# Optimization experiments

Hardware: AMD Instinct MI355X
Metric: run time of the kernel (lower is better)

## Reference

```python
import jax, jax.numpy as jnp
import numpy as np

EXPERT_NUM = 4
TOPK = 2
HIDDEN = 512
B, S = 8, 8192


def setup_inputs() -> dict:
    key = jax.random.key(0)
    k1, k2, k3 = jax.random.split(key, 3)
    x = jax.random.normal(k1, (B, S, HIDDEN), dtype=jnp.float32)
    gate_w = jax.random.normal(k2, (EXPERT_NUM, HIDDEN), dtype=jnp.float32) * (1.0 / np.sqrt(HIDDEN))
    gate_b = jax.random.normal(k3, (EXPERT_NUM,), dtype=jnp.float32) * 0.01
    return {"x": x, "gate_w": gate_w, "gate_b": gate_b}


def reference(x, gate_w, gate_b):
    # logits: [B, S, E]
    logits = jnp.einsum("bsh,eh->bse", x, gate_w) + gate_b
    logits_topk, indices = jax.lax.top_k(logits, TOPK)  # [B,S,K]
    # scatter topk logits into -inf-filled tensor, then softmax over experts
    T = B * S
    flat_logits_topk = logits_topk.reshape(T, TOPK)
    flat_indices = indices.reshape(T, TOPK)
    neg_inf = jnp.full((T, EXPERT_NUM), -jnp.inf, dtype=logits.dtype)
    sparse = neg_inf.at[jnp.arange(T)[:, None], flat_indices].set(flat_logits_topk)
    sparse_logits = jax.nn.softmax(sparse, axis=-1).reshape(B, S, EXPERT_NUM)
    gate_logit = logits.reshape(-1, EXPERT_NUM)  # [B*S, E]
    return sparse_logits, indices, gate_logit
```

## Files before the change

### kernel.cpp

```cpp
#include <hip/hip_runtime.h>
#include <math.h>

#define HIDDEN  512
#define EXPERTS 4

__global__ __launch_bounds__(256, 4) void gating_kernel(
    const float* __restrict__ x,
    const float* __restrict__ gate_w,
    const float* __restrict__ gate_b,
    float* __restrict__ out_sparse,
    float* __restrict__ out_idx,
    float* __restrict__ out_logit,
    int T)
{
    const int lane   = threadIdx.x & 63;
    const int wave   = (int)((blockIdx.x * blockDim.x + threadIdx.x) >> 6);
    const int nwaves = (int)((gridDim.x * blockDim.x) >> 6);

    float4 gw0[EXPERTS], gw1[EXPERTS];
#pragma unroll
    for (int e = 0; e < EXPERTS; ++e) {
        gw0[e] = *reinterpret_cast<const float4*>(gate_w + e * HIDDEN + lane * 4);
        gw1[e] = *reinterpret_cast<const float4*>(gate_w + e * HIDDEN + 256 + lane * 4);
    }
    const float b0 = gate_b[0], b1 = gate_b[1], b2 = gate_b[2], b3 = gate_b[3];

    for (int t = wave; t < T; t += nwaves) {
        const float* xt = x + (size_t)t * HIDDEN;
        const float4 xv0 = *reinterpret_cast<const float4*>(xt + lane * 4);
        const float4 xv1 = *reinterpret_cast<const float4*>(xt + 256 + lane * 4);

        float s[EXPERTS];
#pragma unroll
        for (int e = 0; e < EXPERTS; ++e) {
            s[e] = xv0.x * gw0[e].x + xv0.y * gw0[e].y + xv0.z * gw0[e].z + xv0.w * gw0[e].w
                 + xv1.x * gw1[e].x + xv1.y * gw1[e].y + xv1.z * gw1[e].z + xv1.w * gw1[e].w;
        }

#pragma unroll
        for (int off = 32; off >= 1; off >>= 1) {
#pragma unroll
            for (int e = 0; e < EXPERTS; ++e)
                s[e] += __shfl_xor(s[e], off, 64);
        }

        const float l0 = s[0] + b0, l1 = s[1] + b1, l2 = s[2] + b2, l3 = s[3] + b3;
        const float l[4] = {l0, l1, l2, l3};

        int i1 = 0; float m1 = l[0];
#pragma unroll
        for (int e = 1; e < 4; ++e) { if (l[e] > m1) { m1 = l[e]; i1 = e; } }
        int i2 = -1; float m2 = -INFINITY;
#pragma unroll
        for (int e = 0; e < 4; ++e) { if (e != i1 && l[e] > m2) { m2 = l[e]; i2 = e; } }

        const float e2  = expf(m2 - m1);
        const float inv = 1.0f / (1.0f + e2);
        const float p1  = inv, p2 = e2 * inv;

        float sp[4];
#pragma unroll
        for (int e = 0; e < 4; ++e)
            sp[e] = (e == i1) ? p1 : ((e == i2) ? p2 : 0.0f);

        if (lane == 0) {
            const float4 spv = {sp[0], sp[1], sp[2], sp[3]};
            *reinterpret_cast<float4*>(out_sparse + (size_t)t * 4) = spv;
            const float2 iv = {(float)i1, (float)i2};
            *reinterpret_cast<float2*>(out_idx + (size_t)t * 2) = iv;
            const float4 lv = {l0, l1, l2, l3};
            *reinterpret_cast<float4*>(out_logit + (size_t)t * 4) = lv;
        }
    }
}

extern "C" void kernel_launch(void* const* d_in, const int* in_sizes, int n_in,
                              void* d_out, int out_size, void* d_ws, size_t ws_size,
                              hipStream_t stream) {
    const float* x      = (const float*)d_in[0];
    const float* gate_w = (const float*)d_in[1];
    const float* gate_b = (const float*)d_in[2];

    const int T = in_sizes[0] / HIDDEN;

    float* out_sparse = (float*)d_out;
    float* out_idx    = out_sparse + (size_t)T * EXPERTS;
    float* out_logit  = out_idx    + (size_t)T * 2;

    const dim3 block(256);
    const dim3 grid(1024);
    gating_kernel<<<grid, block, 0, stream>>>(x, gate_w, gate_b,
                                              out_sparse, out_idx, out_logit, T);
}
```

Measured before the change: 191.9 us.

## Process four tokens per wave with transpose-style butterfly reduction

Each wave now loads four token rows at once and keeps more loads in flight. The reduction first shuffles pairs of expert partial sums so that each lane holds one expert's partial. Only one value per token then goes through the remaining xor stages, which cuts the shuffle count per token from 24 to about 10. The result is redistributed with a few extra shuffles, and a tail loop handles leftover tokens. The aim is to hide memory latency in this bandwidth-bound kernel, at the cost of higher register pressure.

```diff
diff --git a/kernel.cpp b/kernel.cpp
--- a/kernel.cpp
+++ b/kernel.cpp
@@ -3,6 +3,7 @@
 
 #define HIDDEN  512
 #define EXPERTS 4
+#define QUAD    4
 
 __global__ __launch_bounds__(256, 4) void gating_kernel(
     const float* __restrict__ x,
@@ -24,52 +25,147 @@
         gw1[e] = *reinterpret_cast<const float4*>(gate_w + e * HIDDEN + 256 + lane * 4);
     }
     const float b0 = gate_b[0], b1 = gate_b[1], b2 = gate_b[2], b3 = gate_b[3];
+    const int id = lane & 3;
 
-    for (int t = wave; t < T; t += nwaves) {
+    const int nquads = T >> 2;
+
+    for (int q = wave; q < nquads; q += nwaves) {
+        const int t0 = q * 4;
+
+        float4 xv0[QUAD], xv1[QUAD];
+#pragma unroll
+        for (int j = 0; j < QUAD; ++j) {
+            const float* xt = x + (size_t)(t0 + j) * HIDDEN;
+            xv0[j] = *reinterpret_cast<const float4*>(xt + lane * 4);
+            xv1[j] = *reinterpret_cast<const float4*>(xt + 256 + lane * 4);
+        }
+
+        float s[QUAD][EXPERTS];
+#pragma unroll
+        for (int j = 0; j < QUAD; ++j) {
+#pragma unroll
+            for (int e = 0; e < EXPERTS; ++e) {
+                s[j][e] = xv0[j].x * gw0[e].x + xv0[j].y * gw0[e].y
+                        + xv0[j].z * gw0[e].z + xv0[j].w * gw0[e].w
+                        + xv1[j].x * gw1[e].x + xv1[j].y * gw1[e].y
+                        + xv1[j].z * gw1[e].z + xv1[j].w * gw1[e].w;
+            }
+        }
+
+        float u[QUAD], v[QUAD];
+#pragma unroll
+        for (int j = 0; j < QUAD; ++j) {
+            float snd = (lane & 1) ? s[j][0] : s[j][1];
+            float rcv = __shfl_xor(snd, 1, 64);
+            u[j] = ((lane & 1) ? s[j][1] : s[j][0]) + rcv;
+        }
+#pragma unroll
+        for (int j = 0; j < QUAD; ++j) {
+            float snd = (lane & 1) ? s[j][2] : s[j][3];
+            float rcv = __shfl_xor(snd, 1, 64);
+            v[j] = ((lane & 1) ? s[j][3] : s[j][2]) + rcv;
+        }
+
+        float r[QUAD];
+#pragma unroll
+        for (int j = 0; j < QUAD; ++j) {
+            float snd = (lane & 2) ? u[j] : v[j];
+            float rcv = __shfl_xor(snd, 2, 64);
+            r[j] = ((lane & 2) ? v[j] : u[j]) + rcv;
+        }
+
+#pragma unroll
+        for (int j = 0; j < QUAD; ++j) r[j] += __shfl_xor(r[j], 4, 64);
+#pragma unroll
+        for (int j = 0; j < QUAD; ++j) r[j] += __shfl_xor(r[j], 8, 64);
+#pragma unroll
+        for (int j = 0; j < QUAD; ++j) r[j] += __shfl_xor(r[j], 16, 64);
+#pragma unroll
+        for (int j = 0; j < QUAD; ++j) r[j] += __shfl_xor(r[j], 32, 64);
+
+        float ga[QUAD], gb[QUAD], gc[QUAD];
+#pragma unroll
+        for (int j = 0; j < QUAD; ++j) ga[j] = __shfl_xor(r[j], 1, 64);
+#pragma unroll
+        for (int j = 0; j < QUAD; ++j) gb[j] = __shfl_xor(r[j], 2, 64);
+#pragma unroll
+        for (int j = 0; j < QUAD; ++j) gc[j] = __shfl_xor(ga[j], 2, 64);
+
+#pragma unroll
+        for (int j = 0; j < QUAD; ++j) {
+            float l_[4];
+#pragma unroll
+            for (int e = 0; e < 4; ++e) {
+                const int m = e ^ id;
+                const float t01 = (m & 1) ? ga[j] : r[j];
+                const float t23 = (m & 1) ? gc[j] : gb[j];
+                l_[e] = (m & 2) ? t23 : t01;
+            }
+            l_[0] += b0; l_[1] += b1; l_[2] += b2; l_[3] += b3;
+
+            int i1 = 0; float m1 = l_[0];
+#pragma unroll
+            for (int e = 1; e < 4; ++e) { if (l_[e] > m1) { m1 = l_[e]; i1 = e; } }
+            int i2 = -1; float m2 = -INFINITY;
+#pragma unroll
+            for (int e = 0; e < 4; ++e) { if (e != i1 && l_[e] > m2) { m2 = l_[e]; i2 = e; } }
+
+            const float e2  = expf(m2 - m1);
+            const float inv = 1.0f / (1.0f + e2);
+            const float p1  = inv, p2 = e2 * inv;
+
+            if (lane == 0) {
+                float sp[4];
+#pragma unroll
+                for (int e = 0; e < 4; ++e)
+                    sp[e] = (e == i1) ? p1 : ((e == i2) ? p2 : 0.0f);
+                const int t = t0 + j;
+                *reinterpret_cast<float4*>(out_sparse + (size_t)t * 4) =
+                    make_float4(sp[0], sp[1], sp[2], sp[3]);
+                *reinterpret_cast<float2*>(out_idx + (size_t)t * 2) =
+                    make_float2((float)i1, (float)i2);
+                *reinterpret_cast<float4*>(out_logit + (size_t)t * 4) =
+                    make_float4(l_[0], l_[1], l_[2], l_[3]);
+            }
+        }
+    }
+
+    for (int t = (nquads << 2) + wave; t < T; t += nwaves) {
         const float* xt = x + (size_t)t * HIDDEN;
-        const float4 xv0 = *reinterpret_cast<const float4*>(xt + lane * 4);
-        const float4 xv1 = *reinterpret_cast<const float4*>(xt + 256 + lane * 4);
-
+        const float4 xa = *reinterpret_cast<const float4*>(xt + lane * 4);
+        const float4 xb = *reinterpret_cast<const float4*>(xt + 256 + lane * 4);
         float s[EXPERTS];
 #pragma unroll
         for (int e = 0; e < EXPERTS; ++e) {
-            s[e] = xv0.x * gw0[e].x + xv0.y * gw0[e].y + xv0.z * gw0[e].z + xv0.w * gw0[e].w
-                 + xv1.x * gw1[e].x + xv1.y * gw1[e].y + xv1.z * gw1[e].z + xv1.w * gw1[e].w;
+            s[e] = xa.x * gw0[e].x + xa.y * gw0[e].y + xa.z * gw0[e].z + xa.w * gw0[e].w
+                 + xb.x * gw1[e].x + xb.y * gw1[e].y + xb.z * gw1[e].z + xb.w * gw1[e].w;
         }
-
 #pragma unroll
         for (int off = 32; off >= 1; off >>= 1) {
 #pragma unroll
-            for (int e = 0; e < EXPERTS; ++e)
-                s[e] += __shfl_xor(s[e], off, 64);
+            for (int e = 0; e < EXPERTS; ++e) s[e] += __shfl_xor(s[e], off, 64);
         }
-
-        const float l0 = s[0] + b0, l1 = s[1] + b1, l2 = s[2] + b2, l3 = s[3] + b3;
-        const float l[4] = {l0, l1, l2, l3};
-
-        int i1 = 0; float m1 = l[0];
+        const float l_[4] = {s[0] + b0, s[1] + b1, s[2] + b2, s[3] + b3};
+        int i1 = 0; float m1 = l_[0];
 #pragma unroll
-        for (int e = 1; e < 4; ++e) { if (l[e] > m1) { m1 = l[e]; i1 = e; } }
+        for (int e = 1; e < 4; ++e) { if (l_[e] > m1) { m1 = l_[e]; i1 = e; } }
         int i2 = -1; float m2 = -INFINITY;
 #pragma unroll
-        for (int e = 0; e < 4; ++e) { if (e != i1 && l[e] > m2) { m2 = l[e]; i2 = e; } }
-
+        for (int e = 0; e < 4; ++e) { if (e != i1 && l_[e] > m2) { m2 = l_[e]; i2 = e; } }
         const float e2  = expf(m2 - m1);
         const float inv = 1.0f / (1.0f + e2);
         const float p1  = inv, p2 = e2 * inv;
-
-        float sp[4];
+        if (lane == 0) {
+            float sp[4];
 #pragma unroll
-        for (int e = 0; e < 4; ++e)
-            sp[e] = (e == i1) ? p1 : ((e == i2) ? p2 : 0.0f);
-
-        if (lane == 0) {
-            const float4 spv = {sp[0], sp[1], sp[2], sp[3]};
-            *reinterpret_cast<float4*>(out_sparse + (size_t)t * 4) = spv;
-            const float2 iv = {(float)i1, (float)i2};
-            *reinterpret_cast<float2*>(out_idx + (size_t)t * 2) = iv;
-            const float4 lv = {l0, l1, l2, l3};
-            *reinterpret_cast<float4*>(out_logit + (size_t)t * 4) = lv;
+            for (int e = 0; e < 4; ++e)
+                sp[e] = (e == i1) ? p1 : ((e == i2) ? p2 : 0.0f);
+            *reinterpret_cast<float4*>(out_sparse + (size_t)t * 4) =
+                make_float4(sp[0], sp[1], sp[2], sp[3]);
+            *reinterpret_cast<float2*>(out_idx + (size_t)t * 2) =
+                make_float2((float)i1, (float)i2);
+            *reinterpret_cast<float4*>(out_logit + (size_t)t * 4) =
+                make_float4(l_[0], l_[1], l_[2], l_[3]);
         }
     }
 }
```

New measurement: 191.6 us. Within noise of the previous version (-0.2%).
